# Kernel optimization log

Measured on AMD Instinct MI355X. Metric: run time of the kernel, lower is better.

Reference implementation:

```python
import jax, jax.numpy as jnp
import numpy as np

N = 100000   # nodes
E = 1600000  # edges (avg degree 16)
D_IN = 128
H = 256
D_OUT = 128


def setup_inputs() -> dict:
    key = jax.random.key(0)
    ks = jax.random.split(key, 12)

    def lin_w(k, fan_in, fan_out):
        # torch nn.Linear-style uniform init
        bound = 1.0 / np.sqrt(fan_in)
        return jax.random.uniform(k, (fan_in, fan_out), jnp.float32, -bound, bound)

    return {
        "in_feat": jax.random.normal(ks[0], (N, D_IN), jnp.float32),
        "src": jax.random.randint(ks[1], (E,), 0, N, jnp.int32),
        "dst": jax.random.randint(ks[2], (E,), 0, N, jnp.int32),
        "Wc0": lin_w(ks[3], D_IN, H), "bc0": jnp.zeros((H,), jnp.float32),
        "Wc1": lin_w(ks[4], H, H),    "bc1": jnp.zeros((H,), jnp.float32),
        "Wc2": lin_w(ks[5], H, D_OUT),"bc2": jnp.zeros((D_OUT,), jnp.float32),
        "Wr0": lin_w(ks[6], D_OUT, H),"br0": jnp.zeros((H,), jnp.float32),
        "Wr1": lin_w(ks[7], H, H),    "br1": jnp.zeros((H,), jnp.float32),
        "Wr2": lin_w(ks[8], H, D_IN), "br2": jnp.zeros((D_IN,), jnp.float32),
    }


def _graph_conv(h, src, dst, W, b):
    """DGL GraphConv, norm='both': D_out^{-1/2} A D_in^{-1/2} h W + b."""
    ones = jnp.ones(src.shape[0], h.dtype)
    out_deg = jnp.clip(jax.ops.segment_sum(ones, src, num_segments=N), 1.0)
    in_deg = jnp.clip(jax.ops.segment_sum(ones, dst, num_segments=N), 1.0)
    h = h * (out_deg ** -0.5)[:, None]
    h = h @ W                                    # transform before aggregate
    h = jax.ops.segment_sum(h[src], dst, num_segments=N)  # SpMM aggregation
    return h * (in_deg ** -0.5)[:, None] + b


def reference(in_feat, src, dst, Wc0, bc0, Wc1, bc1, Wc2, bc2,
              Wr0, br0, Wr1, br1, Wr2, br2):
    h = jnp.tanh(_graph_conv(in_feat, src, dst, Wc0, bc0))
    h = jnp.tanh(_graph_conv(h, src, dst, Wc1, bc1))
    h = jax.nn.softmax(_graph_conv(h, src, dst, Wc2, bc2), axis=1)
    r = jnp.tanh(h @ Wr0 + br0)
    r = jnp.tanh(r @ Wr1 + br1)
    r = jax.nn.softmax(r @ Wr2 + br2, axis=1)
    return (h, r)
```

## Files before the change

kernel.cpp:

```cpp
#include <hip/hip_runtime.h>

typedef __attribute__((ext_vector_type(8))) short short8;
typedef __attribute__((ext_vector_type(4))) float f32x4;

__device__ __forceinline__ ushort f2bf(float v) {
    unsigned u = __builtin_bit_cast(unsigned, v);
    unsigned r = (u + 0x7FFFu + ((u >> 16) & 1u)) >> 16;
    return (ushort)r;
}
__device__ __forceinline__ float lo16(unsigned p) { return __builtin_bit_cast(float, p << 16); }
__device__ __forceinline__ float hi16(unsigned p) { return __builtin_bit_cast(float, p & 0xFFFF0000u); }

__device__ __forceinline__ float fast_tanh(float x) {
    float cx = fminf(fmaxf(x, -9.f), 9.f);
    float e = __expf(2.f * cx);
    return (e - 1.f) / (e + 1.f);
}

__device__ __forceinline__ void async16(const void* g, void* l) {
    __builtin_amdgcn_global_load_lds(
        (const __attribute__((address_space(1))) unsigned*)g,
        (__attribute__((address_space(3))) unsigned*)l, 16, 0, 0);
}

#define BSHIFT 9
#define CHUNK 4096

__global__ __launch_bounds__(256) void bucket_count(const int* __restrict__ src,
        const int* __restrict__ dst, int* __restrict__ gbc,
        int* __restrict__ outc, int E) {
    __shared__ int cnt[256];
    int t = threadIdx.x;
    cnt[t] = 0;
    __syncthreads();
    int start = blockIdx.x * CHUNK;
    int n = E - start; if (n > CHUNK) n = CHUNK;
#pragma unroll
    for (int k = 0; k < CHUNK / 256; ++k) {
        int i = t + k * 256;
        if (i < n) {
            atomicAdd(&cnt[dst[start + i] >> BSHIFT], 1);
            atomicAdd(&outc[src[start + i]], 1);
        }
    }
    __syncthreads();
    if (cnt[t]) atomicAdd(&gbc[t], cnt[t]);
}

__global__ void scan_buckets(const int* __restrict__ gbc, int* __restrict__ bucketBase,
                             int* __restrict__ pairCursor, int* __restrict__ roff,
                             int N, int E) {
    __shared__ int s[256];
    int t = threadIdx.x;
    int v = gbc[t];
    s[t] = v; __syncthreads();
    for (int o = 1; o < 256; o <<= 1) {
        int y = (t >= o) ? s[t - o] : 0;
        __syncthreads();
        s[t] += y;
        __syncthreads();
    }
    int excl = s[t] - v;
    bucketBase[t] = excl;
    pairCursor[t] = excl;
    if (t == 255) bucketBase[256] = s[255];
    if (t == 0) roff[N] = E;
}

__global__ __launch_bounds__(256) void part_scatter(const int* __restrict__ src,
        const int* __restrict__ dst, int* __restrict__ pairCursor,
        uint2* __restrict__ pairs, int E) {
    __shared__ int cnt[256];
    __shared__ int base[256];
    int t = threadIdx.x;
    cnt[t] = 0;
    __syncthreads();
    int start = blockIdx.x * CHUNK;
    int n = E - start; if (n > CHUNK) n = CHUNK;
    int sv[CHUNK / 256], dv[CHUNK / 256], rk[CHUNK / 256], bk[CHUNK / 256];
#pragma unroll
    for (int k = 0; k < CHUNK / 256; ++k) {
        int i = t + k * 256;
        if (i < n) {
            sv[k] = src[start + i];
            dv[k] = dst[start + i];
            bk[k] = dv[k] >> BSHIFT;
            rk[k] = atomicAdd(&cnt[bk[k]], 1);
        } else bk[k] = -1;
    }
    __syncthreads();
    base[t] = cnt[t] ? atomicAdd(&pairCursor[t], cnt[t]) : 0;
    __syncthreads();
#pragma unroll
    for (int k = 0; k < CHUNK / 256; ++k)
        if (bk[k] >= 0) pairs[base[bk[k]] + rk[k]] = make_uint2((unsigned)sv[k], (unsigned)dv[k]);
}

__global__ __launch_bounds__(256) void build_bucket(const uint2* __restrict__ pairs,
        const int* __restrict__ bucketBase, int* __restrict__ roff,
        float* __restrict__ sIn, int* __restrict__ csr, int N) {
    __shared__ int cnt[512];
    __shared__ int cur[512];
    __shared__ int ss[256];
    int b = blockIdx.x;
    int t = threadIdx.x;
    int lo = b << BSHIFT;
    int s0 = bucketBase[b], s1 = bucketBase[b + 1];
    cnt[t] = 0; cnt[t + 256] = 0;
    __syncthreads();
    for (int j = s0 + t; j < s1; j += 256)
        atomicAdd(&cnt[pairs[j].y - lo], 1);
    __syncthreads();
    int c0 = cnt[2 * t], c1 = cnt[2 * t + 1];
    ss[t] = c0 + c1; __syncthreads();
    for (int o = 1; o < 256; o <<= 1) {
        int y = (t >= o) ? ss[t - o] : 0;
        __syncthreads();
        ss[t] += y;
        __syncthreads();
    }
    int eb = ss[t] - (c0 + c1);
    int p0 = s0 + eb, p1 = s0 + eb + c0;
    cur[2 * t] = p0; cur[2 * t + 1] = p1;
    int n0 = lo + 2 * t, n1 = n0 + 1;
    if (n0 < N) { roff[n0] = p0; sIn[n0] = rsqrtf((float)(c0 > 0 ? c0 : 1)); }
    if (n1 < N) { roff[n1] = p1; sIn[n1] = rsqrtf((float)(c1 > 0 ? c1 : 1)); }
    __syncthreads();
    for (int j = s0 + t; j < s1; j += 256) {
        uint2 p = pairs[j];
        int pos = atomicAdd(&cur[p.y - lo], 1);
        csr[pos] = (int)p.x;
    }
}

__global__ void convw(const float* w0, const float* w1, const float* w2,
                      const float* w3, const float* w4, const float* w5,
                      ushort* __restrict__ Wt) {
    int i = blockIdx.x * 256 + threadIdx.x;
    int base, Km, Nm; const float* W;
    if      (i < 32768)  { base = 0;      Km = 128; Nm = 256; W = w0; }
    else if (i < 98304)  { base = 32768;  Km = 256; Nm = 256; W = w1; }
    else if (i < 131072) { base = 98304;  Km = 256; Nm = 128; W = w2; }
    else if (i < 163840) { base = 131072; Km = 128; Nm = 256; W = w3; }
    else if (i < 229376) { base = 163840; Km = 256; Nm = 256; W = w4; }
    else                 { base = 229376; Km = 256; Nm = 128; W = w5; }
    int l = i - base;
    int k = l / Nm, n = l % Nm;
    Wt[base + n * Km + k] = f2bf(W[l]);
}

__global__ void prescale(const float* __restrict__ x, const int* __restrict__ outc,
                         ushort* __restrict__ o, float* __restrict__ sOut,
                         int total ) {
    int i = blockIdx.x * 256 + threadIdx.x;
    if (i >= total) return;
    int row = i >> 5;
    int oc = outc[row]; if (oc < 1) oc = 1;
    float s = rsqrtf((float)oc);
    if ((i & 31) == 0) sOut[row] = s;
    float4 v = ((const float4*)x)[i];
    ushort4 r;
    r.x = f2bf(v.x * s); r.y = f2bf(v.y * s);
    r.z = f2bf(v.z * s); r.w = f2bf(v.w * s);
    ((ushort4*)o)[i] = r;
}


__global__ __launch_bounds__(256) void agg128(const ushort* __restrict__ F,
        const int* __restrict__ csr, const int* __restrict__ roff,
        const float* __restrict__ sIn, ushort* __restrict__ out, int N) {
    int w = blockIdx.x * 4 + (threadIdx.x >> 6);
    if (w >= N) return;
    int lane = threadIdx.x & 63;
    int b = roff[w], e = roff[w + 1];
    int deg = e - b;
    int n = deg < 64 ? deg : 64;
    float a0 = 0.f, a1 = 0.f;
    const char* base = (const char*)(F + lane * 2);
    int voff = 0;
    if (n > 0) voff = csr[b + (lane < n ? lane : n - 1)] << 8;
    int j = 0;
    for (; j + 8 <= n; j += 8) {
        unsigned p[8];
#pragma unroll
        for (int k = 0; k < 8; ++k) {
            int o = __shfl(voff, j + k, 64);
            p[k] = *(const unsigned*)(base + (size_t)(unsigned)o);
        }
#pragma unroll
        for (int k = 0; k < 8; ++k) { a0 += lo16(p[k]); a1 += hi16(p[k]); }
    }
    for (; j < n; ++j) {
        int o = __shfl(voff, j, 64);
        unsigned p = *(const unsigned*)(base + (size_t)(unsigned)o);
        a0 += lo16(p); a1 += hi16(p);
    }
    for (int i = b + 64; i < e; ++i) {
        unsigned p = *(const unsigned*)(base + ((size_t)csr[i] << 8));
        a0 += lo16(p); a1 += hi16(p);
    }
    float s = sIn[w];
    ushort2 o2; o2.x = f2bf(a0 * s); o2.y = f2bf(a1 * s);
    *(ushort2*)(out + (size_t)w * 128 + lane * 2) = o2;
}

__global__ __launch_bounds__(256) void agg256(const ushort* __restrict__ F,
        const int* __restrict__ csr, const int* __restrict__ roff,
        const float* __restrict__ sIn, ushort* __restrict__ out, int N) {
    int w = blockIdx.x * 4 + (threadIdx.x >> 6);
    if (w >= N) return;
    int lane = threadIdx.x & 63;
    int b = roff[w], e = roff[w + 1];
    int deg = e - b;
    int n = deg < 64 ? deg : 64;
    float a0 = 0.f, a1 = 0.f, a2 = 0.f, a3 = 0.f;
    const char* base = (const char*)(F + lane * 4);
    int voff = 0;
    if (n > 0) voff = csr[b + (lane < n ? lane : n - 1)] << 9;
    int j = 0;
    for (; j + 8 <= n; j += 8) {
        uint2 p[8];
#pragma unroll
        for (int k = 0; k < 8; ++k) {
            int o = __shfl(voff, j + k, 64);
            p[k] = *(const uint2*)(base + (size_t)(unsigned)o);
        }
#pragma unroll
        for (int k = 0; k < 8; ++k) {
            a0 += lo16(p[k].x); a1 += hi16(p[k].x);
            a2 += lo16(p[k].y); a3 += hi16(p[k].y);
        }
    }
    for (; j < n; ++j) {
        int o = __shfl(voff, j, 64);
        uint2 p = *(const uint2*)(base + (size_t)(unsigned)o);
        a0 += lo16(p.x); a1 += hi16(p.x); a2 += lo16(p.y); a3 += hi16(p.y);
    }
    for (int i = b + 64; i < e; ++i) {
        uint2 p = *(const uint2*)(base + ((size_t)csr[i] << 9));
        a0 += lo16(p.x); a1 += hi16(p.x); a2 += lo16(p.y); a3 += hi16(p.y);
    }
    float s = sIn[w];
    ushort4 o4;
    o4.x = f2bf(a0 * s); o4.y = f2bf(a1 * s);
    o4.z = f2bf(a2 * s); o4.w = f2bf(a3 * s);
    *(ushort4*)(out + (size_t)w * 256 + lane * 4) = o4;
}

__global__ __launch_bounds__(256) void agg_softmax(const ushort* __restrict__ F,
        const int* __restrict__ csr, const int* __restrict__ roff,
        const float* __restrict__ sIn, const float* __restrict__ bias,
        float* __restrict__ outh, ushort* __restrict__ outb, int N) {
    int w = blockIdx.x * 4 + (threadIdx.x >> 6);
    if (w >= N) return;
    int lane = threadIdx.x & 63;
    int b = roff[w], e = roff[w + 1];
    int deg = e - b;
    int n = deg < 64 ? deg : 64;
    float a0 = 0.f, a1 = 0.f;
    const char* base = (const char*)(F + lane * 2);
    int voff = 0;
    if (n > 0) voff = csr[b + (lane < n ? lane : n - 1)] << 8;
    int j = 0;
    for (; j + 8 <= n; j += 8) {
        unsigned p[8];
#pragma unroll
        for (int k = 0; k < 8; ++k) {
            int o = __shfl(voff, j + k, 64);
            p[k] = *(const unsigned*)(base + (size_t)(unsigned)o);
        }
#pragma unroll
        for (int k = 0; k < 8; ++k) { a0 += lo16(p[k]); a1 += hi16(p[k]); }
    }
    for (; j < n; ++j) {
        int o = __shfl(voff, j, 64);
        unsigned p = *(const unsigned*)(base + (size_t)(unsigned)o);
        a0 += lo16(p); a1 += hi16(p);
    }
    for (int i = b + 64; i < e; ++i) {
        unsigned p = *(const unsigned*)(base + ((size_t)csr[i] << 8));
        a0 += lo16(p); a1 += hi16(p);
    }
    float s = sIn[w];
    float2 bb = *(const float2*)(bias + lane * 2);
    float l0 = a0 * s + bb.x, l1 = a1 * s + bb.y;
    float m = fmaxf(l0, l1);
    for (int o = 32; o; o >>= 1) m = fmaxf(m, __shfl_xor(m, o, 64));
    float e0 = __expf(l0 - m), e1 = __expf(l1 - m);
    float sm = e0 + e1;
    for (int o = 32; o; o >>= 1) sm += __shfl_xor(sm, o, 64);
    float inv = 1.f / sm;
    float r0 = e0 * inv, r1 = e1 * inv;
    float2 fo; fo.x = r0; fo.y = r1;
    *(float2*)(outh + (size_t)w * 128 + lane * 2) = fo;
    ushort2 o2; o2.x = f2bf(r0); o2.y = f2bf(r1);
    *(ushort2*)(outb + (size_t)w * 128 + lane * 2) = o2;
}

template <int MODE>
__global__ __launch_bounds__(256) void gemm_kernel(
        const ushort* __restrict__ A, const ushort* __restrict__ Wt,
        const float* __restrict__ bias, const float* __restrict__ rowscale,
        void* __restrict__ out, int M, int K, int Nn) {
    __shared__ ushort ldsA[128 * 64];
    __shared__ ushort ldsB[128 * 64];
    const int tid = threadIdx.x;
    const int lane = tid & 63;
    const int wid = tid >> 6;
    const int rowbase = blockIdx.x * 128;
    const int colbase = blockIdx.y * 128;
    const int wr = (wid >> 1) * 64;
    const int wc = (wid & 1) * 64;

    f32x4 acc[4][4];
#pragma unroll
    for (int i = 0; i < 4; ++i)
#pragma unroll
        for (int j = 0; j < 4; ++j) acc[i][j] = (f32x4){0.f, 0.f, 0.f, 0.f};

    const int sr = lane >> 3;
    const int sp = lane & 7;

    for (int kt = 0; kt < K; kt += 64) {
        __syncthreads();
#pragma unroll
        for (int it = 0; it < 4; ++it) {
            int rl = wid * 32 + it * 8 + sr;
            int grow = rowbase + rl; if (grow > M - 1) grow = M - 1;
            int gca = kt + ((sp ^ (rl & 7)) << 3);
            async16(A + (size_t)grow * K + gca, (char*)ldsA + (wid * 32 + it * 8) * 128);
            int gn = colbase + rl;
            int gcb = kt + ((sp ^ (rl & 7)) << 3);
            async16(Wt + (size_t)gn * K + gcb, (char*)ldsB + (wid * 32 + it * 8) * 128);
        }
        __syncthreads();
        const int l15 = lane & 15, l4 = lane >> 4;
#pragma unroll
        for (int ks = 0; ks < 2; ++ks) {
            short8 af[4], bfr[4];
#pragma unroll
            for (int rt = 0; rt < 4; ++rt) {
                int r = wr + rt * 16 + l15;
                int slot = (ks * 4 + l4) ^ (r & 7);
                af[rt] = *(const short8*)&ldsA[r * 64 + slot * 8];
            }
#pragma unroll
            for (int ct = 0; ct < 4; ++ct) {
                int n = wc + ct * 16 + l15;
                int slot = (ks * 4 + l4) ^ (n & 7);
                bfr[ct] = *(const short8*)&ldsB[n * 64 + slot * 8];
            }
#pragma unroll
            for (int rt = 0; rt < 4; ++rt)
#pragma unroll
                for (int ct = 0; ct < 4; ++ct)
                    acc[rt][ct] = __builtin_amdgcn_mfma_f32_16x16x32_bf16(
                        af[rt], bfr[ct], acc[rt][ct], 0, 0, 0);
        }
    }

    const int l15 = lane & 15, l4 = lane >> 4;
    float bv[4];
#pragma unroll
    for (int ct = 0; ct < 4; ++ct)
        bv[ct] = (MODE != 1 && bias) ? bias[colbase + wc + ct * 16 + l15] : 0.f;

    if (MODE != 3) {
#pragma unroll
        for (int rt = 0; rt < 4; ++rt) {
#pragma unroll
            for (int rg = 0; rg < 4; ++rg) {
                int row = rowbase + wr + rt * 16 + l4 * 4 + rg;
                if (row >= M) continue;
                float sc = 1.f;
                if (MODE == 0 && rowscale) sc = rowscale[row];
#pragma unroll
                for (int ct = 0; ct < 4; ++ct) {
                    int col = colbase + wc + ct * 16 + l15;
                    float v = acc[rt][ct][rg] + bv[ct];
                    if (MODE == 0) v = fast_tanh(v) * sc;
                    if (MODE <= 1)
                        ((ushort*)out)[(size_t)row * Nn + col] = f2bf(v);
                    else
                        ((float*)out)[(size_t)row * Nn + col] = v;
                }
            }
        }
    } else {
        __syncthreads();
        float* sred = (float*)ldsA;
#pragma unroll
        for (int rt = 0; rt < 4; ++rt) {
#pragma unroll
            for (int rg = 0; rg < 4; ++rg) {
                float m = acc[rt][0][rg] + bv[0];
#pragma unroll
                for (int ct = 1; ct < 4; ++ct) m = fmaxf(m, acc[rt][ct][rg] + bv[ct]);
                m = fmaxf(m, __shfl_xor(m, 1, 64));
                m = fmaxf(m, __shfl_xor(m, 2, 64));
                m = fmaxf(m, __shfl_xor(m, 4, 64));
                m = fmaxf(m, __shfl_xor(m, 8, 64));
                int row = wr + rt * 16 + l4 * 4 + rg;
                if (l15 == 0) sred[(wid & 1) * 128 + row] = m;
            }
        }
        __syncthreads();
#pragma unroll
        for (int rt = 0; rt < 4; ++rt) {
#pragma unroll
            for (int rg = 0; rg < 4; ++rg) {
                int row = wr + rt * 16 + l4 * 4 + rg;
                float m = fmaxf(sred[row], sred[128 + row]);
                float s = 0.f;
#pragma unroll
                for (int ct = 0; ct < 4; ++ct) {
                    float ev = __expf(acc[rt][ct][rg] + bv[ct] - m);
                    acc[rt][ct][rg] = ev;
                    s += ev;
                }
                s += __shfl_xor(s, 1, 64);
                s += __shfl_xor(s, 2, 64);
                s += __shfl_xor(s, 4, 64);
                s += __shfl_xor(s, 8, 64);
                if (l15 == 0) sred[256 + (wid & 1) * 128 + row] = s;
            }
        }
        __syncthreads();
#pragma unroll
        for (int rt = 0; rt < 4; ++rt) {
#pragma unroll
            for (int rg = 0; rg < 4; ++rg) {
                int row = wr + rt * 16 + l4 * 4 + rg;
                float inv = 1.f / (sred[256 + row] + sred[256 + 128 + row]);
                int grow = rowbase + row;
                if (grow >= M) continue;
#pragma unroll
                for (int ct = 0; ct < 4; ++ct) {
                    int col = colbase + wc + ct * 16 + l15;
                    ((float*)out)[(size_t)grow * Nn + col] = acc[rt][ct][rg] * inv;
                }
            }
        }
    }
}

extern "C" void kernel_launch(void* const* d_in, const int* in_sizes, int n_in,
                              void* d_out, int out_size, void* d_ws, size_t ws_size,
                              hipStream_t stream) {
    (void)n_in; (void)out_size; (void)ws_size;
    const float* in_feat = (const float*)d_in[0];
    const int*   src     = (const int*)d_in[1];
    const int*   dstp    = (const int*)d_in[2];
    const float* Wc0 = (const float*)d_in[3];  const float* bc0 = (const float*)d_in[4];
    const float* Wc1 = (const float*)d_in[5];  const float* bc1 = (const float*)d_in[6];
    const float* Wc2 = (const float*)d_in[7];  const float* bc2 = (const float*)d_in[8];
    const float* Wr0 = (const float*)d_in[9];  const float* br0 = (const float*)d_in[10];
    const float* Wr1 = (const float*)d_in[11]; const float* br1 = (const float*)d_in[12];
    const float* Wr2 = (const float*)d_in[13]; const float* br2 = (const float*)d_in[14];

    const int N = in_sizes[0] / 128;
    const int E = in_sizes[1];
    const int numBuckets = (N + ((1 << BSHIFT) - 1)) >> BSHIFT;

    char* ws = (char*)d_ws;
    size_t off = 0;
    auto alloc = [&](size_t bytes) -> char* {
        char* p = ws + off;
        off += (bytes + 255) & ~(size_t)255;
        return p;
    };
    char* S1 = alloc((size_t)N * 256 * 2);
    char* S2 = alloc((size_t)N * 256 * 2);
    int* csr    = (int*)alloc((size_t)E * 4);
    int* roff   = (int*)alloc((size_t)(N + 1) * 4);
    int* outc   = (int*)alloc((size_t)N * 4);
    float* sOut = (float*)alloc((size_t)N * 4);
    float* sIn  = (float*)alloc((size_t)N * 4);
    ushort* Wt  = (ushort*)alloc(262144 * 2);
    int* gbc        = (int*)alloc(256 * 4);
    int* bucketBase = (int*)alloc(257 * 4);
    int* pairCursor = (int*)alloc(256 * 4);
    uint2* pairs = (uint2*)S2;

    hipMemsetAsync(outc, 0, (size_t)N * 4, stream);
    hipMemsetAsync(gbc, 0, 256 * 4, stream);

    int nblk = (E + CHUNK - 1) / CHUNK;
    bucket_count<<<nblk, 256, 0, stream>>>(src, dstp, gbc, outc, E);
    scan_buckets<<<1, 256, 0, stream>>>(gbc, bucketBase, pairCursor, roff, N, E);
    part_scatter<<<nblk, 256, 0, stream>>>(src, dstp, pairCursor, pairs, E);
    build_bucket<<<numBuckets, 256, 0, stream>>>(pairs, bucketBase, roff, sIn, csr, N);

    convw<<<262144 / 256, 256, 0, stream>>>(Wc0, Wc1, Wc2, Wr0, Wr1, Wr2, Wt);

    ushort* Xs = (ushort*)S1;
    prescale<<<(N * 32 + 255) / 256, 256, 0, stream>>>(in_feat, outc, Xs, sOut, N * 32);

    int aggGrid = (N + 3) / 4;
    dim3 g2((N + 127) / 128, 2), g1((N + 127) / 128, 1);

    ushort* A0 = (ushort*)S2;
    agg128<<<aggGrid, 256, 0, stream>>>(Xs, csr, roff, sIn, A0, N);
    ushort* B1 = (ushort*)S1;
    gemm_kernel<0><<<g2, 256, 0, stream>>>(A0, Wt, bc0, sOut, B1, N, 128, 256);
    ushort* A1 = (ushort*)S2;
    agg256<<<aggGrid, 256, 0, stream>>>(B1, csr, roff, sIn, A1, N);
    ushort* B2 = (ushort*)S1;
    gemm_kernel<0><<<g2, 256, 0, stream>>>(A1, Wt + 32768, bc1, sOut, B2, N, 256, 256);
    ushort* T3 = (ushort*)S2;
    gemm_kernel<1><<<g1, 256, 0, stream>>>(B2, Wt + 98304, nullptr, nullptr, T3, N, 256, 128);
    float* outh = (float*)d_out;
    ushort* Hbf = (ushort*)S1;
    agg_softmax<<<aggGrid, 256, 0, stream>>>(T3, csr, roff, sIn, bc2, outh, Hbf, N);
    ushort* R1 = (ushort*)S2;
    gemm_kernel<0><<<g2, 256, 0, stream>>>(Hbf, Wt + 131072, br0, nullptr, R1, N, 128, 256);
    ushort* R2 = (ushort*)S1;
    gemm_kernel<0><<<g2, 256, 0, stream>>>(R1, Wt + 163840, br1, nullptr, R2, N, 256, 256);
    gemm_kernel<3><<<g1, 256, 0, stream>>>(R2, Wt + 229376, br2, nullptr,
                                           outh + (size_t)N * 128, N, 256, 128);
}
```

Baseline: 735.9 us.

## Replace row-per-wave SpMM aggregation with column-sliced edge-parallel aggregation

The per-layer aggregation kernels are replaced by a templated kernel that splits the feature dimension into 32-byte column slices. Each wave handles 16 rows, with 8 edges processed in parallel per row and each group of 8 lanes reading one slice, then reducing across lanes with shuffles. Interleaving slice indices across blocks is meant to keep each slice's working set of gathered rows small enough to stay cache-resident, and non-temporal loads and stores are used for index and output streams. In exchange, csr and roff are re-read once per slice and the 256-wide layer needs two launches. Only 8 of 64 lanes issue stores, and the shuffle reductions add work per row.

```diff
diff --git a/kernel.cpp b/kernel.cpp
--- a/kernel.cpp
+++ b/kernel.cpp
@@ -165,86 +165,42 @@
     ((ushort4*)o)[i] = r;
 }
 
-
-__global__ __launch_bounds__(256) void agg128(const ushort* __restrict__ F,
+template <int RB>
+__global__ __launch_bounds__(256) void agg_slice(const ushort* __restrict__ F,
         const int* __restrict__ csr, const int* __restrict__ roff,
-        const float* __restrict__ sIn, ushort* __restrict__ out, int N) {
-    int w = blockIdx.x * 4 + (threadIdx.x >> 6);
-    if (w >= N) return;
-    int lane = threadIdx.x & 63;
-    int b = roff[w], e = roff[w + 1];
-    int deg = e - b;
-    int n = deg < 64 ? deg : 64;
-    float a0 = 0.f, a1 = 0.f;
-    const char* base = (const char*)(F + lane * 2);
-    int voff = 0;
-    if (n > 0) voff = csr[b + (lane < n ? lane : n - 1)] << 8;
-    int j = 0;
-    for (; j + 8 <= n; j += 8) {
-        unsigned p[8];
-#pragma unroll
-        for (int k = 0; k < 8; ++k) {
-            int o = __shfl(voff, j + k, 64);
-            p[k] = *(const unsigned*)(base + (size_t)(unsigned)o);
-        }
-#pragma unroll
-        for (int k = 0; k < 8; ++k) { a0 += lo16(p[k]); a1 += hi16(p[k]); }
-    }
-    for (; j < n; ++j) {
-        int o = __shfl(voff, j, 64);
-        unsigned p = *(const unsigned*)(base + (size_t)(unsigned)o);
-        a0 += lo16(p); a1 += hi16(p);
-    }
-    for (int i = b + 64; i < e; ++i) {
-        unsigned p = *(const unsigned*)(base + ((size_t)csr[i] << 8));
-        a0 += lo16(p); a1 += hi16(p);
-    }
-    float s = sIn[w];
-    ushort2 o2; o2.x = f2bf(a0 * s); o2.y = f2bf(a1 * s);
-    *(ushort2*)(out + (size_t)w * 128 + lane * 2) = o2;
-}
-
-__global__ __launch_bounds__(256) void agg256(const ushort* __restrict__ F,
-        const int* __restrict__ csr, const int* __restrict__ roff,
-        const float* __restrict__ sIn, ushort* __restrict__ out, int N) {
-    int w = blockIdx.x * 4 + (threadIdx.x >> 6);
-    if (w >= N) return;
-    int lane = threadIdx.x & 63;
-    int b = roff[w], e = roff[w + 1];
-    int deg = e - b;
-    int n = deg < 64 ? deg : 64;
-    float a0 = 0.f, a1 = 0.f, a2 = 0.f, a3 = 0.f;
-    const char* base = (const char*)(F + lane * 4);
-    int voff = 0;
-    if (n > 0) voff = csr[b + (lane < n ? lane : n - 1)] << 9;
-    int j = 0;
-    for (; j + 8 <= n; j += 8) {
-        uint2 p[8];
-#pragma unroll
-        for (int k = 0; k < 8; ++k) {
-            int o = __shfl(voff, j + k, 64);
-            p[k] = *(const uint2*)(base + (size_t)(unsigned)o);
-        }
-#pragma unroll
-        for (int k = 0; k < 8; ++k) {
-            a0 += lo16(p[k].x); a1 += hi16(p[k].x);
-            a2 += lo16(p[k].y); a3 += hi16(p[k].y);
-        }
-    }
-    for (; j < n; ++j) {
-        int o = __shfl(voff, j, 64);
-        uint2 p = *(const uint2*)(base + (size_t)(unsigned)o);
-        a0 += lo16(p.x); a1 += hi16(p.x); a2 += lo16(p.y); a3 += hi16(p.y);
-    }
-    for (int i = b + 64; i < e; ++i) {
-        uint2 p = *(const uint2*)(base + ((size_t)csr[i] << 9));
-        a0 += lo16(p.x); a1 += hi16(p.x); a2 += lo16(p.y); a3 += hi16(p.y);
-    }
-    float s = sIn[w];
-    ushort4 o4;
-    o4.x = f2bf(a0 * s); o4.y = f2bf(a1 * s);
-    o4.z = f2bf(a2 * s); o4.w = f2bf(a3 * s);
-    *(ushort4*)(out + (size_t)w * 256 + lane * 4) = o4;
+        const float* __restrict__ sIn, ushort* __restrict__ out,
+        int sliceBase, int rowsPerWave, int N) {
+    const int s = (blockIdx.x & 7) + sliceBase;
+    const int wv = (blockIdx.x >> 3) * 4 + (threadIdx.x >> 6);
+    const int lane = threadIdx.x & 63;
+    const int e8 = lane >> 3;
+    const int d  = lane & 7;
+    int r0 = wv * rowsPerWave;
+    if (r0 >= N) return;
+    int r1 = r0 + rowsPerWave; if (r1 > N) r1 = N;
+    const char* Fs = (const char*)F + s * 32 + d * 4;
+    for (int r = r0; r < r1; ++r) {
+        int b = __builtin_nontemporal_load(&roff[r]);
+        int e = __builtin_nontemporal_load(&roff[r + 1]);
+        float a0 = 0.f, a1 = 0.f;
+        for (int i = b; i < e; i += 8) {
+            int ii = i + e8;
+            if (ii < e) {
+                int idx = __builtin_nontemporal_load(&csr[ii]);
+                unsigned p = *(const unsigned*)(Fs + (size_t)idx * RB);
+                a0 += lo16(p); a1 += hi16(p);
+            }
+        }
+        a0 += __shfl_xor(a0, 8, 64);  a1 += __shfl_xor(a1, 8, 64);
+        a0 += __shfl_xor(a0, 16, 64); a1 += __shfl_xor(a1, 16, 64);
+        a0 += __shfl_xor(a0, 32, 64); a1 += __shfl_xor(a1, 32, 64);
+        float sc = sIn[r];
+        if (lane < 8) {
+            ushort2 o2; o2.x = f2bf(a0 * sc); o2.y = f2bf(a1 * sc);
+            __builtin_nontemporal_store(__builtin_bit_cast(unsigned, o2),
+                (unsigned*)((char*)out + (size_t)r * RB + s * 32 + d * 4));
+        }
+    }
 }
 
 __global__ __launch_bounds__(256) void agg_softmax(const ushort* __restrict__ F,
@@ -499,12 +455,17 @@
     int aggGrid = (N + 3) / 4;
     dim3 g2((N + 127) / 128, 2), g1((N + 127) / 128, 1);
 
+    const int RPW = 16;
+    int slBlocks = (N + 4 * RPW - 1) / (4 * RPW);
+    dim3 gs(slBlocks * 8);
+
     ushort* A0 = (ushort*)S2;
-    agg128<<<aggGrid, 256, 0, stream>>>(Xs, csr, roff, sIn, A0, N);
+    agg_slice<256><<<gs, 256, 0, stream>>>(Xs, csr, roff, sIn, A0, 0, RPW, N);
     ushort* B1 = (ushort*)S1;
     gemm_kernel<0><<<g2, 256, 0, stream>>>(A0, Wt, bc0, sOut, B1, N, 128, 256);
     ushort* A1 = (ushort*)S2;
-    agg256<<<aggGrid, 256, 0, stream>>>(B1, csr, roff, sIn, A1, N);
+    agg_slice<512><<<gs, 256, 0, stream>>>(B1, csr, roff, sIn, A1, 0, RPW, N);
+    agg_slice<512><<<gs, 256, 0, stream>>>(B1, csr, roff, sIn, A1, 8, RPW, N);
     ushort* B2 = (ushort*)S1;
     gemm_kernel<0><<<g2, 256, 0, stream>>>(A1, Wt + 32768, bc1, sOut, B2, N, 256, 256);
     ushort* T3 = (ushort*)S2;
```

After: 1.805 ms. 2.45x slower.
